# Kernel optimization log

Hardware: AMD Instinct MI355X
Metric: run time of the kernel (lower is better)

Reference implementation:

```python
import jax, jax.numpy as jnp
import numpy as np

N = 100_000      # nodes
E = 3_200_000    # edges (avg degree 32)
IN = 128         # input feature dim
H1, C1 = 8, 8    # layer-1 heads, channels per head (concat -> 64)
OUT = 2          # output classes (layer-2: 1 head, mean/no-concat)
NEG = 0.2        # LeakyReLU negative slope (PyG default)


def setup_inputs() -> dict:
    key = jax.random.key(0)
    ks = jax.random.split(key, 11)
    s1 = 1.0 / np.sqrt(IN)
    s2 = 1.0 / np.sqrt(H1 * C1)
    return {
        "x": jax.random.normal(ks[0], (N, IN), jnp.float32),
        "edge_index": jax.random.randint(ks[1], (2, E), 0, N, dtype=jnp.int32),
        "edge_attr": jax.random.normal(ks[2], (E, 1), jnp.float32),
        "W1": jax.random.normal(ks[3], (IN, H1 * C1), jnp.float32) * s1,
        "a1_src": jax.random.normal(ks[4], (H1, C1), jnp.float32) * s1,
        "a1_dst": jax.random.normal(ks[5], (H1, C1), jnp.float32) * s1,
        "b1": jnp.zeros((H1 * C1,), jnp.float32),
        "W2": jax.random.normal(ks[6], (H1 * C1, OUT), jnp.float32) * s2,
        "a2_src": jax.random.normal(ks[7], (1, OUT), jnp.float32) * s2,
        "a2_dst": jax.random.normal(ks[8], (1, OUT), jnp.float32) * s2,
        "b2": jnp.zeros((OUT,), jnp.float32),
    }


def gat_conv(x, W, a_src, a_dst, b, src, dst, heads, ch, concat):
    """PyG GATConv: per-head linear, per-edge LeakyReLU attention, segment softmax over dst."""
    n = x.shape[0]
    h = (x @ W).reshape(n, heads, ch)                 # [N, H, C]
    al_src = jnp.sum(h * a_src, axis=-1)              # [N, H]
    al_dst = jnp.sum(h * a_dst, axis=-1)              # [N, H]
    e = al_src[src] + al_dst[dst]                     # [Etot, H]
    e = jnp.where(e > 0, e, NEG * e)                  # LeakyReLU
    m = jax.lax.stop_gradient(jax.ops.segment_max(e, dst, num_segments=n))
    ex = jnp.exp(e - m[dst])
    den = jax.ops.segment_sum(ex, dst, num_segments=n)
    alpha = ex / den[dst]                             # segment softmax
    out = jax.ops.segment_sum(alpha[:, :, None] * h[src], dst, num_segments=n)  # [N, H, C]
    out = out.reshape(n, heads * ch) if concat else out.mean(axis=1)
    return out + b


def reference(x, edge_index, edge_attr, W1, a1_src, a1_dst, b1, W2, a2_src, a2_dst, b2):
    # add_self_loops=True (PyG default)
    loops = jnp.arange(x.shape[0], dtype=edge_index.dtype)
    src = jnp.concatenate([edge_index[0], loops])
    dst = jnp.concatenate([edge_index[1], loops])
    h = gat_conv(x, W1, a1_src, a1_dst, b1, src, dst, H1, C1, True)
    h = jax.nn.elu(h)
    return gat_conv(h, W2, a2_src, a2_dst, b2, src, dst, 1, OUT, False)
```

## Files before the change

kernel.cpp:

```cpp
#include <hip/hip_runtime.h>
#include <math.h>

#define NNODES 100000
#define NEDGES 3200000
#define ETOT   (NEDGES + NNODES)
#define IN_DIM 128
#define NH1    8
#define NC1    8
#define HC     64
#define OUTC   2
#define NEGSL  0.2f
#define L2E    1.44269504f

#define NBUCK 391
#define EPB   2048
#define NBLK  1563
#define TOTC  (NBUCK * NBLK)


__global__ __launch_bounds__(256) void histA(const int* __restrict__ ei,
                                             int* __restrict__ carr) {
    __shared__ int lh[NBUCK];
    int tid = threadIdx.x;
    for (int i = tid; i < NBUCK; i += 256) lh[i] = 0;
    __syncthreads();
    const int* dptr = ei + NEDGES;
    int base = blockIdx.x * EPB;
#pragma unroll
    for (int i = 0; i < EPB / 1024; i++) {
        int idx = base + i * 1024 + tid * 4;
        if (idx < NEDGES) {
            int4 d4 = *(const int4*)&dptr[idx];
            atomicAdd(&lh[d4.x >> 8], 1);
            atomicAdd(&lh[d4.y >> 8], 1);
            atomicAdd(&lh[d4.z >> 8], 1);
            atomicAdd(&lh[d4.w >> 8], 1);
        }
    }
    __syncthreads();
    for (int i = tid; i < NBUCK; i += 256)
        carr[i * NBLK + blockIdx.x] = lh[i];
}

__global__ __launch_bounds__(256) void scanA(int* __restrict__ carr,
                                             int* __restrict__ bsums) {
    int gid = blockIdx.x * 256 + threadIdx.x;
    int v = (gid < TOTC) ? carr[gid] : 0;
    int lane = threadIdx.x & 63, w = threadIdx.x >> 6;
    int x = v;
    for (int off = 1; off < 64; off <<= 1) {
        int y = __shfl_up(x, off, 64);
        if (lane >= off) x += y;
    }
    __shared__ int wt[4];
    if (lane == 63) wt[w] = x;
    __syncthreads();
    int add = 0;
    for (int i = 0; i < w; i++) add += wt[i];
    int incl = x + add;
    if (gid < TOTC) carr[gid] = incl - v;
    if (threadIdx.x == 255) bsums[blockIdx.x] = incl;
}

__global__ __launch_bounds__(1024) void scanB(int* __restrict__ bsums, int nb) {
    int tid = threadIdx.x;
    int base = tid * 4;
    int v[4]; int tot = 0;
#pragma unroll
    for (int j = 0; j < 4; j++) {
        v[j] = (base + j < nb) ? bsums[base + j] : 0;
        tot += v[j];
    }
    int lane = tid & 63, w = tid >> 6;
    int x = tot;
    for (int off = 1; off < 64; off <<= 1) {
        int y = __shfl_up(x, off, 64);
        if (lane >= off) x += y;
    }
    __shared__ int wt[16];
    if (lane == 63) wt[w] = x;
    __syncthreads();
    int add = 0;
    for (int i = 0; i < w; i++) add += wt[i];
    int pre = x + add - tot;
#pragma unroll
    for (int j = 0; j < 4; j++) {
        if (base + j < nb) bsums[base + j] = pre;
        pre += v[j];
    }
}

__global__ __launch_bounds__(256) void scanC(int* __restrict__ carr,
                                             const int* __restrict__ bsums) {
    int gid = blockIdx.x * 256 + threadIdx.x;
    if (gid < TOTC) carr[gid] += bsums[gid >> 8];
}

__global__ __launch_bounds__(256) void scatC(const int* __restrict__ ei,
                                             const int* __restrict__ soff,
                                             int* __restrict__ ebuf) {
    __shared__ int soffL[NBUCK];
    __shared__ int lh[NBUCK];
    int tid = threadIdx.x;
    for (int i = tid; i < NBUCK; i += 256) {
        soffL[i] = soff[i * NBLK + blockIdx.x];
        lh[i] = 0;
    }
    __syncthreads();
    int base = blockIdx.x * EPB;
#pragma unroll
    for (int i = 0; i < EPB / 1024; i++) {
        int idx = base + i * 1024 + tid * 4;
        if (idx < NEDGES) {
            int4 s4 = *(const int4*)&ei[idx];
            int4 d4 = *(const int4*)&ei[NEDGES + idx];
            int b0 = d4.x >> 8, b1 = d4.y >> 8, b2 = d4.z >> 8, b3 = d4.w >> 8;
            int r0 = atomicAdd(&lh[b0], 1);
            int r1 = atomicAdd(&lh[b1], 1);
            int r2 = atomicAdd(&lh[b2], 1);
            int r3 = atomicAdd(&lh[b3], 1);
            ebuf[soffL[b0] + r0] = s4.x | ((d4.x & 255) << 17);
            ebuf[soffL[b1] + r1] = s4.y | ((d4.y & 255) << 17);
            ebuf[soffL[b2] + r2] = s4.z | ((d4.z & 255) << 17);
            ebuf[soffL[b3] + r3] = s4.w | ((d4.w & 255) << 17);
        }
    }
}

__global__ __launch_bounds__(256) void buildD(const int* __restrict__ soff,
                                              const int* __restrict__ ebuf,
                                              int* __restrict__ rowoff,
                                              int* __restrict__ srcs) {
    int b = blockIdx.x, tid = threadIdx.x;
    int nb = min(256, NNODES - b * 256);
    int ebeg = soff[b * NBLK];
    int eend = (b == NBUCK - 1) ? NEDGES : soff[(b + 1) * NBLK];
    __shared__ int cnt2[256];
    __shared__ int rowL[256];
    __shared__ int wsum[4];
    cnt2[tid] = 0;
    __syncthreads();
    for (int e = ebeg + tid; e < eend; e += 256)
        atomicAdd(&cnt2[(ebuf[e] >> 17) & 255], 1);
    __syncthreads();
    int v = (tid < nb) ? cnt2[tid] + 1 : 0;
    int lane = tid & 63, w = tid >> 6;
    int x = v;
    for (int off = 1; off < 64; off <<= 1) {
        int y = __shfl_up(x, off, 64);
        if (lane >= off) x += y;
    }
    if (lane == 63) wsum[w] = x;
    __syncthreads();
    int add = 0;
    for (int i = 0; i < w; i++) add += wsum[i];
    int fbase = ebeg + b * 256;
    int row = fbase + x + add - v;
    if (tid < nb) {
        rowL[tid] = row;
        int gnode = b * 256 + tid;
        rowoff[gnode] = row;
        srcs[row + cnt2[tid]] = gnode;
        if (gnode == NNODES - 1) rowoff[NNODES] = ETOT;
    }
    __syncthreads();
    cnt2[tid] = 0;
    __syncthreads();
    for (int e = ebeg + tid; e < eend; e += 256) {
        int wv = ebuf[e];
        int dl = (wv >> 17) & 255;
        int r = atomicAdd(&cnt2[dl], 1);
        srcs[rowL[dl] + r] = wv & 0x1FFFF;
    }
}


__global__ __launch_bounds__(256) void gemm1(const float* __restrict__ x,
                                             const float* __restrict__ W1,
                                             const float* __restrict__ a1s,
                                             const float* __restrict__ a1d,
                                             unsigned short* __restrict__ h1b,
                                             float2* __restrict__ alE,
                                             float* __restrict__ al1d) {
    __shared__ float sW[IN_DIM * HC];
    int tid = threadIdx.x;
    const float4* W4 = (const float4*)W1;
    float4* sW4 = (float4*)sW;
#pragma unroll
    for (int i = 0; i < 8; i++)
        sW4[tid + i * 256] = W4[tid + i * 256];
    __syncthreads();

    int w = __builtin_amdgcn_readfirstlane(tid >> 6);
    int lane = tid & 63;
    int node0 = blockIdx.x * 16 + w * 4;
    const float* xr = x + (size_t)node0 * IN_DIM;

    float acc0 = 0.f, acc1 = 0.f, acc2 = 0.f, acc3 = 0.f;
#pragma unroll 8
    for (int k = 0; k < IN_DIM; k++) {
        float wv = sW[k * HC + lane];
        acc0 = fmaf(xr[k], wv, acc0);
        acc1 = fmaf(xr[IN_DIM + k], wv, acc1);
        acc2 = fmaf(xr[2 * IN_DIM + k], wv, acc2);
        acc3 = fmaf(xr[3 * IN_DIM + k], wv, acc3);
    }

    float accs[4] = {acc0, acc1, acc2, acc3};
    int head = lane >> 3, c = lane & 7;
    float as = a1s[head * NC1 + c], adv = a1d[head * NC1 + c];
#pragma unroll
    for (int n = 0; n < 4; n++) {
        int node = node0 + n;
        unsigned int u = __float_as_uint(accs[n]);
        h1b[node * HC + lane] =
            (unsigned short)((u + 0x7FFF + ((u >> 16) & 1)) >> 16);
        float ps = accs[n] * as;
        float pd = accs[n] * adv;
        for (int off = 1; off < 8; off <<= 1) {
            ps += __shfl_xor(ps, off, 64);
            pd += __shfl_xor(pd, off, 64);
        }
        if (c == 0) {
            alE[node * NH1 + head] = make_float2(exp2f(ps * L2E),
                                                 exp2f(ps * (NEGSL * L2E)));
            al1d[node * NH1 + head] = pd;
        }
    }
}


__global__ __launch_bounds__(256) void agg1(const unsigned short* __restrict__ h1b,
                                            const float2* __restrict__ alE,
                                            const float* __restrict__ al1d,
                                            const float* __restrict__ b1,
                                            const float* __restrict__ W2,
                                            const float* __restrict__ a2s,
                                            const float* __restrict__ a2d,
                                            const int* __restrict__ rowoff,
                                            const int* __restrict__ srcs,
                                            float4* __restrict__ nd2,
                                            float* __restrict__ al2d) {
    int w = threadIdx.x >> 6, lane = threadIdx.x & 63;
    int node = blockIdx.x * 4 + w;
    if (node >= NNODES) return;
    int h = lane >> 3;
    float ald = al1d[node * NH1 + h];
    float E1d = exp2f(ald * L2E);
    float E2d = exp2f(ald * (NEGSL * L2E));
    int beg = __builtin_amdgcn_readfirstlane(rowoff[node]);
    int end = __builtin_amdgcn_readfirstlane(rowoff[node + 1]);

    float den = 0.f, acc = 0.f, denB = 0.f, accB = 0.f;
    int i = beg;
    for (; i + 4 <= end; i += 4) {
        int s0 = __builtin_amdgcn_readfirstlane(srcs[i]);
        int s1 = __builtin_amdgcn_readfirstlane(srcs[i + 1]);
        int s2 = __builtin_amdgcn_readfirstlane(srcs[i + 2]);
        int s3 = __builtin_amdgcn_readfirstlane(srcs[i + 3]);
        float2 e0 = alE[s0 * NH1 + h];
        float2 e1 = alE[s1 * NH1 + h];
        float2 e2 = alE[s2 * NH1 + h];
        float2 e3 = alE[s3 * NH1 + h];
        float hv0 = __uint_as_float((unsigned int)h1b[s0 * HC + lane] << 16);
        float hv1 = __uint_as_float((unsigned int)h1b[s1 * HC + lane] << 16);
        float hv2 = __uint_as_float((unsigned int)h1b[s2 * HC + lane] << 16);
        float hv3 = __uint_as_float((unsigned int)h1b[s3 * HC + lane] << 16);
        float p0 = fmaxf(e0.x * E1d, e0.y * E2d);
        float p1 = fmaxf(e1.x * E1d, e1.y * E2d);
        float p2 = fmaxf(e2.x * E1d, e2.y * E2d);
        float p3 = fmaxf(e3.x * E1d, e3.y * E2d);
        den  += p0;  acc  = fmaf(p0, hv0, acc);
        denB += p1;  accB = fmaf(p1, hv1, accB);
        den  += p2;  acc  = fmaf(p2, hv2, acc);
        denB += p3;  accB = fmaf(p3, hv3, accB);
    }
    for (; i < end; ++i) {
        int s0 = __builtin_amdgcn_readfirstlane(srcs[i]);
        float2 e0 = alE[s0 * NH1 + h];
        float hv0 = __uint_as_float((unsigned int)h1b[s0 * HC + lane] << 16);
        float p0 = fmaxf(e0.x * E1d, e0.y * E2d);
        den += p0; acc = fmaf(p0, hv0, acc);
    }
    den += denB; acc += accB;

    float o = acc / den + b1[lane];
    o = (o > 0.f) ? o : expm1f(o);
    float p0 = o * W2[lane * OUTC + 0];
    float p1 = o * W2[lane * OUTC + 1];
    for (int off = 1; off < 64; off <<= 1) {
        p0 += __shfl_xor(p0, off, 64);
        p1 += __shfl_xor(p1, off, 64);
    }
    if (lane == 0) {
        float l2s = p0 * a2s[0] + p1 * a2s[1];
        float l2d = p0 * a2d[0] + p1 * a2d[1];
        nd2[node] = make_float4(exp2f(l2s * L2E), exp2f(l2s * (NEGSL * L2E)),
                                p0, p1);
        al2d[node] = l2d;
    }
}


__global__ __launch_bounds__(256) void agg2(const float4* __restrict__ nd2,
                                            const float* __restrict__ al2d,
                                            const float* __restrict__ b2,
                                            const int* __restrict__ rowoff,
                                            const int* __restrict__ srcs,
                                            float* __restrict__ out) {
    int w = threadIdx.x >> 6, lane = threadIdx.x & 63;
    int n = blockIdx.x * 4 + w;
    if (n >= NNODES) return;
    float ald = al2d[n];
    float E1d = exp2f(ald * L2E);
    float E2d = exp2f(ald * (NEGSL * L2E));
    int beg = rowoff[n], end = rowoff[n + 1];
    float den = 0.f, a0 = 0.f, a1 = 0.f;
    for (int idx = beg + lane; idx < end; idx += 64) {
        int s = srcs[idx];
        float4 nd = nd2[s];
        float p = fmaxf(nd.x * E1d, nd.y * E2d);
        den += p;
        a0 = fmaf(p, nd.z, a0);
        a1 = fmaf(p, nd.w, a1);
    }
    for (int off = 1; off < 64; off <<= 1) {
        den += __shfl_xor(den, off, 64);
        a0  += __shfl_xor(a0, off, 64);
        a1  += __shfl_xor(a1, off, 64);
    }
    if (lane == 0) {
        out[n * 2 + 0] = a0 / den + b2[0];
        out[n * 2 + 1] = a1 / den + b2[1];
    }
}


extern "C" void kernel_launch(void* const* d_in, const int* in_sizes, int n_in,
                              void* d_out, int out_size, void* d_ws, size_t ws_size,
                              hipStream_t stream) {
    const float* x   = (const float*)d_in[0];
    const int*   ei  = (const int*)  d_in[1];
    const float* W1  = (const float*)d_in[3];
    const float* a1s = (const float*)d_in[4];
    const float* a1d = (const float*)d_in[5];
    const float* b1  = (const float*)d_in[6];
    const float* W2  = (const float*)d_in[7];
    const float* a2s = (const float*)d_in[8];
    const float* a2d = (const float*)d_in[9];
    const float* b2  = (const float*)d_in[10];
    float* out = (float*)d_out;

    char* ws = (char*)d_ws;
    unsigned short* h1b = (unsigned short*)ws;
    float2* alE   = (float2*)(ws + (size_t)NNODES * HC * 2);
    float* al1d_  = (float*)(alE + (size_t)NNODES * NH1);
    float4* nd2   = (float4*)(al1d_ + (size_t)NNODES * NH1);
    float* al2d_  = (float*)(nd2 + NNODES);
    int* rowoff   = (int*)(al2d_ + NNODES);
    int* srcs     = rowoff + NNODES + 1;
    int* ebuf     = (int*)ws;
    int* carr     = ebuf + NEDGES;
    int* bsums    = carr + TOTC;

    const int NB_SC  = (TOTC + 255) / 256;
    const int NB_N4  = (NNODES + 3) / 4;
    const int NB_G   = NNODES / 16;

    histA<<<NBLK, 256, 0, stream>>>(ei, carr);
    scanA<<<NB_SC, 256, 0, stream>>>(carr, bsums);
    scanB<<<1, 1024, 0, stream>>>(bsums, NB_SC);
    scanC<<<NB_SC, 256, 0, stream>>>(carr, bsums);
    scatC<<<NBLK, 256, 0, stream>>>(ei, carr, ebuf);
    buildD<<<NBUCK, 256, 0, stream>>>(carr, ebuf, rowoff, srcs);

    gemm1<<<NB_G, 256, 0, stream>>>(x, W1, a1s, a1d, h1b, alE, al1d_);

    agg1<<<NB_N4, 256, 0, stream>>>(h1b, alE, al1d_, b1, W2, a2s, a2d,
                                    rowoff, srcs, nd2, al2d_);

    agg2<<<NB_N4, 256, 0, stream>>>(nd2, al2d_, b2, rowoff, srcs, out);
}
```

Baseline: 282.2 us.

## Split agg1 wavefront into two half-waves each gathering two channels per edge

The layer-1 aggregation now has each half of a wavefront process a different edge, with every lane loading two bf16 channels as one 32-bit word. Each load instruction therefore covers two edges, halving the number of gather instructions, and the two halves are combined with a cross-half shuffle at the end. The odd-edge tail is handled with a predicated pass. Separately, the histogram kernel processes twice as many edges per block, using half as many blocks. This adds shuffle work and fewer uniform scalar loads, and the tail predication adds some divergence.

After: 268.9 us (median of 4 runs). 4.7% less time.

```diff
diff --git a/kernel.cpp b/kernel.cpp
--- a/kernel.cpp
+++ b/kernel.cpp
@@ -13,8 +13,8 @@
 #define L2E    1.44269504f
 
 #define NBUCK 391
-#define EPB   2048
-#define NBLK  1563
+#define EPB   4096
+#define NBLK  782
 #define TOTC  (NBUCK * NBLK)
 
 
@@ -244,51 +244,60 @@
     int w = threadIdx.x >> 6, lane = threadIdx.x & 63;
     int node = blockIdx.x * 4 + w;
     if (node >= NNODES) return;
-    int h = lane >> 3;
-    float ald = al1d[node * NH1 + h];
+    int ep = lane >> 5;
+    int c  = lane & 31;
+    int hh = c >> 2;
+    float ald = al1d[node * NH1 + hh];
     float E1d = exp2f(ald * L2E);
     float E2d = exp2f(ald * (NEGSL * L2E));
     int beg = __builtin_amdgcn_readfirstlane(rowoff[node]);
     int end = __builtin_amdgcn_readfirstlane(rowoff[node + 1]);
 
-    float den = 0.f, acc = 0.f, denB = 0.f, accB = 0.f;
+    float den = 0.f, acc0 = 0.f, acc1 = 0.f;
+    float denB = 0.f, acc0B = 0.f, acc1B = 0.f;
     int i = beg;
     for (; i + 4 <= end; i += 4) {
-        int s0 = __builtin_amdgcn_readfirstlane(srcs[i]);
-        int s1 = __builtin_amdgcn_readfirstlane(srcs[i + 1]);
-        int s2 = __builtin_amdgcn_readfirstlane(srcs[i + 2]);
-        int s3 = __builtin_amdgcn_readfirstlane(srcs[i + 3]);
-        float2 e0 = alE[s0 * NH1 + h];
-        float2 e1 = alE[s1 * NH1 + h];
-        float2 e2 = alE[s2 * NH1 + h];
-        float2 e3 = alE[s3 * NH1 + h];
-        float hv0 = __uint_as_float((unsigned int)h1b[s0 * HC + lane] << 16);
-        float hv1 = __uint_as_float((unsigned int)h1b[s1 * HC + lane] << 16);
-        float hv2 = __uint_as_float((unsigned int)h1b[s2 * HC + lane] << 16);
-        float hv3 = __uint_as_float((unsigned int)h1b[s3 * HC + lane] << 16);
-        float p0 = fmaxf(e0.x * E1d, e0.y * E2d);
-        float p1 = fmaxf(e1.x * E1d, e1.y * E2d);
-        float p2 = fmaxf(e2.x * E1d, e2.y * E2d);
-        float p3 = fmaxf(e3.x * E1d, e3.y * E2d);
-        den  += p0;  acc  = fmaf(p0, hv0, acc);
-        denB += p1;  accB = fmaf(p1, hv1, accB);
-        den  += p2;  acc  = fmaf(p2, hv2, acc);
-        denB += p3;  accB = fmaf(p3, hv3, accB);
-    }
-    for (; i < end; ++i) {
-        int s0 = __builtin_amdgcn_readfirstlane(srcs[i]);
-        float2 e0 = alE[s0 * NH1 + h];
-        float hv0 = __uint_as_float((unsigned int)h1b[s0 * HC + lane] << 16);
-        float p0 = fmaxf(e0.x * E1d, e0.y * E2d);
-        den += p0; acc = fmaf(p0, hv0, acc);
-    }
-    den += denB; acc += accB;
-
-    float o = acc / den + b1[lane];
-    o = (o > 0.f) ? o : expm1f(o);
-    float p0 = o * W2[lane * OUTC + 0];
-    float p1 = o * W2[lane * OUTC + 1];
-    for (int off = 1; off < 64; off <<= 1) {
+        int sa = srcs[i + ep];
+        int sb = srcs[i + 2 + ep];
+        float2 ea = alE[sa * NH1 + hh];
+        float2 eb = alE[sb * NH1 + hh];
+        unsigned int ha = *(const unsigned int*)&h1b[sa * HC + 2 * c];
+        unsigned int hb = *(const unsigned int*)&h1b[sb * HC + 2 * c];
+        float pa = fmaxf(ea.x * E1d, ea.y * E2d);
+        float pb = fmaxf(eb.x * E1d, eb.y * E2d);
+        float va0 = __uint_as_float(ha << 16);
+        float va1 = __uint_as_float(ha & 0xFFFF0000u);
+        float vb0 = __uint_as_float(hb << 16);
+        float vb1 = __uint_as_float(hb & 0xFFFF0000u);
+        den  += pa;  acc0  = fmaf(pa, va0, acc0);  acc1  = fmaf(pa, va1, acc1);
+        denB += pb;  acc0B = fmaf(pb, vb0, acc0B); acc1B = fmaf(pb, vb1, acc1B);
+    }
+    for (; i < end; i += 2) {
+        int ia = i + ep;
+        bool valid = ia < end;
+        int sa = srcs[valid ? ia : end - 1];
+        float2 ea = alE[sa * NH1 + hh];
+        unsigned int ha = *(const unsigned int*)&h1b[sa * HC + 2 * c];
+        float pa = fmaxf(ea.x * E1d, ea.y * E2d);
+        pa = valid ? pa : 0.f;
+        float va0 = __uint_as_float(ha << 16);
+        float va1 = __uint_as_float(ha & 0xFFFF0000u);
+        den += pa; acc0 = fmaf(pa, va0, acc0); acc1 = fmaf(pa, va1, acc1);
+    }
+    den += denB; acc0 += acc0B; acc1 += acc1B;
+    den  += __shfl_xor(den, 32, 64);
+    acc0 += __shfl_xor(acc0, 32, 64);
+    acc1 += __shfl_xor(acc1, 32, 64);
+
+    float2 b1v = *(const float2*)&b1[2 * c];
+    float o0 = acc0 / den + b1v.x;
+    float o1 = acc1 / den + b1v.y;
+    o0 = (o0 > 0.f) ? o0 : expm1f(o0);
+    o1 = (o1 > 0.f) ? o1 : expm1f(o1);
+    float4 w2v = *(const float4*)&W2[4 * c];
+    float p0 = o0 * w2v.x + o1 * w2v.z;
+    float p1 = o0 * w2v.y + o1 * w2v.w;
+    for (int off = 1; off < 32; off <<= 1) {
         p0 += __shfl_xor(p0, off, 64);
         p1 += __shfl_xor(p1, off, 64);
     }
```

## Split wavefront into four edge groups in layer-1 aggregation with vectorized bf16 loads

Applied to the files above, without the earlier changes.

The layer-1 aggregation kernel now splits each 64-lane wavefront into four 16-lane groups. Each group handles a different edge at the same time, and each lane loads four bf16 channels as a uint2. Source indices are loaded cooperatively 64 at a time and broadcast with shuffles. Attention weights are computed once per head by 8 lanes and shuffled to the others. Partial sums are reduced across groups at the end. The goal is more memory-level parallelism and fewer, wider gather loads per edge, at the cost of extra shuffles and some idle lanes. The histogram block size is also doubled. The early-return node bound check was removed, which is safe only because the node count divides evenly into blocks of four.

After: 273.6 us. -3.1%, faster.

```diff
diff --git a/kernel.cpp b/kernel.cpp
--- a/kernel.cpp
+++ b/kernel.cpp
@@ -13,8 +13,8 @@
 #define L2E    1.44269504f
 
 #define NBUCK 391
-#define EPB   2048
-#define NBLK  1563
+#define EPB   4096
+#define NBLK  782
 #define TOTC  (NBUCK * NBLK)
 
 
@@ -243,52 +243,58 @@
                                             float* __restrict__ al2d) {
     int w = threadIdx.x >> 6, lane = threadIdx.x & 63;
     int node = blockIdx.x * 4 + w;
-    if (node >= NNODES) return;
-    int h = lane >> 3;
-    float ald = al1d[node * NH1 + h];
+    int q = lane & 15;
+    float ald = al1d[node * NH1 + (q & 7)];
     float E1d = exp2f(ald * L2E);
     float E2d = exp2f(ald * (NEGSL * L2E));
     int beg = __builtin_amdgcn_readfirstlane(rowoff[node]);
     int end = __builtin_amdgcn_readfirstlane(rowoff[node + 1]);
-
-    float den = 0.f, acc = 0.f, denB = 0.f, accB = 0.f;
-    int i = beg;
-    for (; i + 4 <= end; i += 4) {
-        int s0 = __builtin_amdgcn_readfirstlane(srcs[i]);
-        int s1 = __builtin_amdgcn_readfirstlane(srcs[i + 1]);
-        int s2 = __builtin_amdgcn_readfirstlane(srcs[i + 2]);
-        int s3 = __builtin_amdgcn_readfirstlane(srcs[i + 3]);
-        float2 e0 = alE[s0 * NH1 + h];
-        float2 e1 = alE[s1 * NH1 + h];
-        float2 e2 = alE[s2 * NH1 + h];
-        float2 e3 = alE[s3 * NH1 + h];
-        float hv0 = __uint_as_float((unsigned int)h1b[s0 * HC + lane] << 16);
-        float hv1 = __uint_as_float((unsigned int)h1b[s1 * HC + lane] << 16);
-        float hv2 = __uint_as_float((unsigned int)h1b[s2 * HC + lane] << 16);
-        float hv3 = __uint_as_float((unsigned int)h1b[s3 * HC + lane] << 16);
-        float p0 = fmaxf(e0.x * E1d, e0.y * E2d);
-        float p1 = fmaxf(e1.x * E1d, e1.y * E2d);
-        float p2 = fmaxf(e2.x * E1d, e2.y * E2d);
-        float p3 = fmaxf(e3.x * E1d, e3.y * E2d);
-        den  += p0;  acc  = fmaf(p0, hv0, acc);
-        denB += p1;  accB = fmaf(p1, hv1, accB);
-        den  += p2;  acc  = fmaf(p2, hv2, acc);
-        denB += p3;  accB = fmaf(p3, hv3, accB);
-    }
-    for (; i < end; ++i) {
-        int s0 = __builtin_amdgcn_readfirstlane(srcs[i]);
-        float2 e0 = alE[s0 * NH1 + h];
-        float hv0 = __uint_as_float((unsigned int)h1b[s0 * HC + lane] << 16);
-        float p0 = fmaxf(e0.x * E1d, e0.y * E2d);
-        den += p0; acc = fmaf(p0, hv0, acc);
-    }
-    den += denB; acc += accB;
-
-    float o = acc / den + b1[lane];
-    o = (o > 0.f) ? o : expm1f(o);
-    float p0 = o * W2[lane * OUTC + 0];
-    float p1 = o * W2[lane * OUTC + 1];
-    for (int off = 1; off < 64; off <<= 1) {
+    int pidx = (lane & 0x30) | (q >> 1);
+
+    float den = 0.f, a0 = 0.f, a1 = 0.f, a2 = 0.f, a3 = 0.f;
+    for (int base = beg; base < end; base += 64) {
+        int idx = base + lane;
+        int sv = srcs[idx < end ? idx : end - 1];
+        int nq = min(16, (end - base + 3) >> 2);
+        for (int t = 0; t < nq; t++) {
+            int s = __shfl(sv, 4 * t + (lane >> 4), 64);
+            float p = 0.f;
+            if (q < 8) {
+                float2 ea = alE[s * NH1 + q];
+                p = fmaxf(ea.x * E1d, ea.y * E2d);
+            }
+            p = __shfl(p, pidx, 64);
+            bool valid = (base + 4 * t + (lane >> 4)) < end;
+            p = valid ? p : 0.f;
+            uint2 hv = *(const uint2*)&h1b[s * HC + 4 * q];
+            den += p;
+            a0 = fmaf(p, __uint_as_float(hv.x << 16), a0);
+            a1 = fmaf(p, __uint_as_float(hv.x & 0xFFFF0000u), a1);
+            a2 = fmaf(p, __uint_as_float(hv.y << 16), a2);
+            a3 = fmaf(p, __uint_as_float(hv.y & 0xFFFF0000u), a3);
+        }
+    }
+    den += __shfl_xor(den, 16, 64);  den += __shfl_xor(den, 32, 64);
+    a0  += __shfl_xor(a0, 16, 64);   a0  += __shfl_xor(a0, 32, 64);
+    a1  += __shfl_xor(a1, 16, 64);   a1  += __shfl_xor(a1, 32, 64);
+    a2  += __shfl_xor(a2, 16, 64);   a2  += __shfl_xor(a2, 32, 64);
+    a3  += __shfl_xor(a3, 16, 64);   a3  += __shfl_xor(a3, 32, 64);
+
+    float rd = 1.f / den;
+    float4 b1v = *(const float4*)&b1[4 * q];
+    float o0 = fmaf(a0, rd, b1v.x);
+    float o1 = fmaf(a1, rd, b1v.y);
+    float o2 = fmaf(a2, rd, b1v.z);
+    float o3 = fmaf(a3, rd, b1v.w);
+    o0 = (o0 > 0.f) ? o0 : expm1f(o0);
+    o1 = (o1 > 0.f) ? o1 : expm1f(o1);
+    o2 = (o2 > 0.f) ? o2 : expm1f(o2);
+    o3 = (o3 > 0.f) ? o3 : expm1f(o3);
+    float4 w2a = *(const float4*)&W2[8 * q];
+    float4 w2b = *(const float4*)&W2[8 * q + 4];
+    float p0 = o0 * w2a.x + o1 * w2a.z + o2 * w2b.x + o3 * w2b.z;
+    float p1 = o0 * w2a.y + o1 * w2a.w + o2 * w2b.y + o3 * w2b.w;
+    for (int off = 1; off < 16; off <<= 1) {
         p0 += __shfl_xor(p0, off, 64);
         p1 += __shfl_xor(p1, off, 64);
     }
```
